# Performance work log

Measured on AMD Instinct MI355X. Metric: run time of the kernel, lower is better.

Reference implementation:

```python
import jax, jax.numpy as jnp
import numpy as np
from jax import lax

B, T, C_IN = 64, 1000, 12
D_MODEL, D_STATE, D_CONV, EXPAND = 128, 16, 4, 2
D_INNER = EXPAND * D_MODEL          # 256
DT_RANK = (D_MODEL + 15) // 16      # ceil(d_model/16) = 8
NUM_CLASSES = 5


def setup_inputs() -> dict:
    key = jax.random.key(0)
    ks = jax.random.split(key, 12)
    s = 0.05
    f = jnp.float32
    return {
        "x": jax.random.normal(ks[0], (B, T, C_IN), f),
        # input projection Linear(C_IN, D_MODEL) with bias
        "ip_w": jax.random.normal(ks[1], (D_MODEL, C_IN), f) * s,
        "ip_b": jnp.zeros((D_MODEL,), f),
        # Mamba block params (mamba_ssm layout)
        "in_proj_w": jax.random.normal(ks[2], (2 * D_INNER, D_MODEL), f) * s,
        "conv_w": jax.random.normal(ks[3], (D_INNER, D_CONV), f) * s,
        "conv_b": jnp.zeros((D_INNER,), f),
        "x_proj_w": jax.random.normal(ks[4], (DT_RANK + 2 * D_STATE, D_INNER), f) * s,
        "dt_proj_w": jax.random.normal(ks[5], (D_INNER, DT_RANK), f) * s,
        "dt_proj_b": jax.random.uniform(ks[6], (D_INNER,), f, -4.0, -2.0),  # softplus -> small positive dt
        "A_log": jnp.log(jnp.tile(jnp.arange(1, D_STATE + 1, dtype=f), (D_INNER, 1))),
        "D_skip": jnp.ones((D_INNER,), f),
        "out_proj_w": jax.random.normal(ks[7], (D_MODEL, D_INNER), f) * s,
        # classifier head: Linear(128,64) -> ReLU -> Linear(64,5)
        "fc1_w": jax.random.normal(ks[8], (64, D_MODEL), f) * s,
        "fc1_b": jnp.zeros((64,), f),
        "fc2_w": jax.random.normal(ks[9], (NUM_CLASSES, 64), f) * s,
        "fc2_b": jnp.zeros((NUM_CLASSES,), f),
    }


def _silu(x):
    return x * jax.nn.sigmoid(x)


def _mamba(h, in_proj_w, conv_w, conv_b, x_proj_w, dt_proj_w, dt_proj_b,
           A_log, D_skip, out_proj_w):
    # h: (B, T, D_MODEL)
    xz = h @ in_proj_w.T                              # (B, T, 2*Di)
    xm, z = jnp.split(xz, 2, axis=-1)
    # depthwise causal conv over time (pad left d_conv-1)
    xp = jnp.pad(xm, ((0, 0), (D_CONV - 1, 0), (0, 0)))
    rhs = conv_w.T[:, None, :]                        # (d_conv, 1, Di)
    xc = lax.conv_general_dilated(
        xp, rhs, (1,), 'VALID',
        dimension_numbers=('NHC', 'HIO', 'NHC'),
        feature_group_count=D_INNER) + conv_b
    u = _silu(xc)                                     # (B, T, Di)
    dbc = u @ x_proj_w.T                              # (B, T, dt_rank + 2N)
    dt = dbc[..., :DT_RANK]
    Bm = dbc[..., DT_RANK:DT_RANK + D_STATE]          # (B, T, N)
    Cm = dbc[..., DT_RANK + D_STATE:]                 # (B, T, N)
    delta = jax.nn.softplus(dt @ dt_proj_w.T + dt_proj_b)  # (B, T, Di)
    A = -jnp.exp(A_log)                               # (Di, N)

    def step(hst, inp):
        d_t, b_t, c_t, u_t = inp                      # (B,Di),(B,N),(B,N),(B,Di)
        dA = jnp.exp(d_t[..., None] * A)              # (B, Di, N)
        hst = dA * hst + (d_t * u_t)[..., None] * b_t[:, None, :]
        y_t = jnp.einsum('bdn,bn->bd', hst, c_t)
        return hst, y_t

    h0 = jnp.zeros((h.shape[0], D_INNER, D_STATE), h.dtype)
    _, ys = lax.scan(step, h0, (delta.transpose(1, 0, 2), Bm.transpose(1, 0, 2),
                                Cm.transpose(1, 0, 2), u.transpose(1, 0, 2)))
    y = ys.transpose(1, 0, 2) + u * D_skip            # (B, T, Di)
    y = y * _silu(z)
    return y @ out_proj_w.T                           # (B, T, D_MODEL)


def reference(x, ip_w, ip_b, in_proj_w, conv_w, conv_b, x_proj_w, dt_proj_w,
              dt_proj_b, A_log, D_skip, out_proj_w, fc1_w, fc1_b, fc2_w, fc2_b):
    h = x @ ip_w.T + ip_b                             # (B, T, D_MODEL)
    y = _mamba(h, in_proj_w, conv_w, conv_b, x_proj_w, dt_proj_w, dt_proj_b,
               A_log, D_skip, out_proj_w)
    last = y[:, -1, :]                                # (B, D_MODEL)
    hid = jax.nn.relu(last @ fc1_w.T + fc1_b)
    return hid @ fc2_w.T + fc2_b                      # (B, NUM_CLASSES)
```

## Files before the change

### kernel.cpp

```cpp
#include <hip/hip_runtime.h>
#include <cstddef>

#define T_LEN 1000
#define B_SZ 64
#define C_IN_ 12
#define D_MODEL_ 128
#define D_INNER_ 256
#define D_STATE_ 16
#define DT_RANK_ 8
#define N_CLS 5
#define NCH 5
#define CT4 50

typedef __attribute__((ext_vector_type(8))) short bf16x8;
typedef __attribute__((ext_vector_type(8))) unsigned short u16x8;
typedef __attribute__((ext_vector_type(4))) float f32x4;

__device__ __forceinline__ float fast_exp2(float x) {
#if __has_builtin(__builtin_amdgcn_exp2f)
  return __builtin_amdgcn_exp2f(x);
#else
  float r; asm volatile("v_exp_f32 %0, %1" : "=v"(r) : "v"(x)); return r;
#endif
}
__device__ __forceinline__ float fast_log2(float x) {
#if __has_builtin(__builtin_amdgcn_logf)
  return __builtin_amdgcn_logf(x);
#else
  float r; asm volatile("v_log_f32 %0, %1" : "=v"(r) : "v"(x)); return r;
#endif
}
__device__ __forceinline__ float fast_rcp(float x) {
#if __has_builtin(__builtin_amdgcn_rcpf)
  return __builtin_amdgcn_rcpf(x);
#else
  float r; asm volatile("v_rcp_f32 %0, %1" : "=v"(r) : "v"(x)); return r;
#endif
}
__device__ __forceinline__ float silu_f(float x) {
  float den = 1.f + fast_exp2(-x * 1.4426950408889634f);
  return x * fast_rcp(den);
}
__device__ __forceinline__ float softplus_f(float x) {
  const float L = 1.4426950408889634f, iL = 0.6931471805599453f;
  float e = fast_exp2(-fabsf(x) * L);
  float l = fast_log2(1.f + e) * iL;
  return fmaxf(x, 0.f) + l;
}
__device__ __forceinline__ unsigned short f2bf(float f) {
  unsigned u = __builtin_bit_cast(unsigned, f);
  u = u + 0x7FFFu + ((u >> 16) & 1u);
  return (unsigned short)(u >> 16);
}
__device__ __forceinline__ float bf2f(unsigned short h) {
  unsigned u = ((unsigned)h) << 16;
  return __builtin_bit_cast(float, u);
}

__global__ __launch_bounds__(256) void k0_prep(
    const float* __restrict__ x, const float* __restrict__ ip_w,
    const float* __restrict__ ip_b, const float* __restrict__ in_proj_w,
    char* __restrict__ h_pk, char* __restrict__ w_pk)
{
  __shared__ unsigned short pk_s[8192];
  __shared__ unsigned short pkw_s[32768];
  const int tid = threadIdx.x;

  if (blockIdx.x == 16) {
    if (blockIdx.y != 0) return;
    const int n = tid;
    for (int k = 0; k < D_MODEL_; ++k) {
      unsigned short v = f2bf(in_proj_w[(size_t)n * D_MODEL_ + k]);
      int off = ((n >> 4) * 4 + (k >> 5)) * 512 + ((k & 31) >> 3) * 128
              + (n & 15) * 8 + (k & 7);
      pkw_s[off] = v;
    }
    __syncthreads();
    const float4* s4 = (const float4*)pkw_s;
    float4* dst = (float4*)w_pk;
#pragma unroll
    for (int q = 0; q < 16; ++q) dst[tid * 16 + q] = s4[tid * 16 + q];
    return;
  }

  const int tile4 = blockIdx.x;
  const int b = blockIdx.y;
  const int rl = tid & 63;
  const int kc = (tid >> 6) * 32;
  const int t = tile4 * 64 + rl;

  float xr[C_IN_] = {0.f, 0.f, 0.f, 0.f, 0.f, 0.f, 0.f, 0.f, 0.f, 0.f, 0.f, 0.f};
  const bool valid = (t < T_LEN);
  if (valid) {
    const float4* xp = (const float4*)(x + ((size_t)b * T_LEN + t) * C_IN_);
    float4 v0 = xp[0], v1 = xp[1], v2 = xp[2];
    xr[0] = v0.x; xr[1] = v0.y; xr[2] = v0.z;  xr[3] = v0.w;
    xr[4] = v1.x; xr[5] = v1.y; xr[6] = v1.z;  xr[7] = v1.w;
    xr[8] = v2.x; xr[9] = v2.y; xr[10] = v2.z; xr[11] = v2.w;
  }
  for (int kk = 0; kk < 32; ++kk) {
    const int k = kc + kk;
    unsigned short v = 0;
    if (valid) {
      float acc = ip_b[k];
      const float* wr = ip_w + k * C_IN_;
#pragma unroll
      for (int c = 0; c < C_IN_; ++c) acc += xr[c] * wr[c];
      v = f2bf(acc);
    }
    int off = (rl >> 4) * 2048 + (k >> 5) * 512 + ((k & 31) >> 3) * 128
            + (rl & 15) * 8 + (k & 7);
    pk_s[off] = v;
  }
  __syncthreads();
  const float4* s4 = (const float4*)pk_s;
  float4* dst = (float4*)(h_pk + (size_t)(b * 64 + tile4 * 4) * 4096);
#pragma unroll
  for (int q = 0; q < 4; ++q) dst[tid * 4 + q] = s4[tid * 4 + q];
}

__global__ __launch_bounds__(256) void k1_u(
    const char* __restrict__ h_pk, const char* __restrict__ w_pk,
    const float* __restrict__ conv_w, const float* __restrict__ conv_b,
    float* __restrict__ u_out)
{
  __shared__ float xm[67][260];

  const int tile = blockIdx.x;
  const int b    = blockIdx.y;
  const int t0   = tile * 64;
  const int tid  = threadIdx.x;
  const int w    = tid >> 6;
  const int l    = tid & 63;

  {
    const char* achunk = h_pk + (size_t)(b * 64 + tile * 4 + w) * 4096;
    bf16x8 a0 = *(const bf16x8*)(achunk + 0 * 1024 + l * 16);
    bf16x8 a1 = *(const bf16x8*)(achunk + 1 * 1024 + l * 16);
    bf16x8 a2 = *(const bf16x8*)(achunk + 2 * 1024 + l * 16);
    bf16x8 a3 = *(const bf16x8*)(achunk + 3 * 1024 + l * 16);

    const int row_l = w * 16 + (l >> 4) * 4;
#pragma unroll
    for (int nt = 0; nt < 16; ++nt) {
      const char* wb = w_pk + (size_t)nt * 4096 + l * 16;
      bf16x8 b0 = *(const bf16x8*)(wb + 0 * 1024);
      bf16x8 b1 = *(const bf16x8*)(wb + 1 * 1024);
      bf16x8 b2 = *(const bf16x8*)(wb + 2 * 1024);
      bf16x8 b3 = *(const bf16x8*)(wb + 3 * 1024);
      f32x4 acc = {0.f, 0.f, 0.f, 0.f};
      acc = __builtin_amdgcn_mfma_f32_16x16x32_bf16(a0, b0, acc, 0, 0, 0);
      acc = __builtin_amdgcn_mfma_f32_16x16x32_bf16(a1, b1, acc, 0, 0, 0);
      acc = __builtin_amdgcn_mfma_f32_16x16x32_bf16(a2, b2, acc, 0, 0, 0);
      acc = __builtin_amdgcn_mfma_f32_16x16x32_bf16(a3, b3, acc, 0, 0, 0);
      const int col = nt * 16 + (l & 15);
#pragma unroll
      for (int r = 0; r < 4; ++r)
        xm[3 + row_l + r][col] = acc[r];
    }
  }

  {
    const int n = tid;
    float hac[3] = {0.f, 0.f, 0.f};
    if (tile > 0) {
      const char* wrow = w_pk + (size_t)(n >> 4) * 4096 + (n & 15) * 16;
#pragma unroll
      for (int kt = 0; kt < 4; ++kt)
#pragma unroll
        for (int lg = 0; lg < 4; ++lg) {
          u16x8 wv = *(const u16x8*)(wrow + kt * 1024 + lg * 256);
#pragma unroll
          for (int r = 0; r < 3; ++r) {
            const int t = t0 - 3 + r;
            const char* hc = h_pk + (size_t)(b * 64 + (t >> 4)) * 4096;
            u16x8 hv = *(const u16x8*)(hc + kt * 1024 + lg * 256 + (t & 15) * 16);
#pragma unroll
            for (int j = 0; j < 8; ++j) hac[r] += bf2f(hv[j]) * bf2f(wv[j]);
          }
        }
    }
#pragma unroll
    for (int r = 0; r < 3; ++r) xm[r][n] = hac[r];
  }
  __syncthreads();

  {
    const int n = tid;
    const float4 cw = *(const float4*)&conv_w[n * 4];
    const float  cb = conv_b[n];
    float x0 = xm[0][n], x1 = xm[1][n], x2 = xm[2][n];
    for (int i = 0; i < 64; ++i) {
      const int t = t0 + i;
      float x3 = xm[3 + i][n];
      if (t < T_LEN) {
        float s = cb + x0 * cw.x + x1 * cw.y + x2 * cw.z + x3 * cw.w;
        u_out[(((size_t)b * T_LEN + t) << 8) + n] = silu_f(s);
      }
      x0 = x1; x1 = x2; x2 = x3;
    }
  }
}

__global__ __launch_bounds__(256) void k3_delta(
    const float* __restrict__ u, const float* __restrict__ x_proj_w,
    const float* __restrict__ dt_proj_w, const float* __restrict__ dt_proj_b,
    float* __restrict__ pk_delta, float* __restrict__ pk_du,
    float* __restrict__ pk_bm, float* __restrict__ u_last)
{
  __shared__ float4 xp4[24][65];
  __shared__ float dt_s[64][9];
  __shared__ float bm_s[64][17];

  const int row0 = blockIdx.x * 64;
  const int tid = threadIdx.x;

  for (int f = tid; f < 24 * 64; f += 256) {
    int c = f >> 6, k4 = f & 63;
    xp4[c][k4] = *(const float4*)&x_proj_w[(size_t)c * 256 + k4 * 4];
  }
  const float4 w0 = *(const float4*)&dt_proj_w[(size_t)tid * 8];
  const float4 w1 = *(const float4*)&dt_proj_w[(size_t)tid * 8 + 4];
  const float bias = dt_proj_b[tid];
  __syncthreads();

  {
    const int r2 = tid >> 3, cg = tid & 7;
    const int ra = 2 * r2;
    const float4* ua4 = (const float4*)(u + (size_t)(row0 + ra) * 256);
    const float4* ub4 = (const float4*)(u + (size_t)(row0 + ra + 1) * 256);
    float a0 = 0.f, a1 = 0.f, a2 = 0.f, b0 = 0.f, b1 = 0.f, b2 = 0.f;
    for (int k4 = 0; k4 < 64; ++k4) {
      float4 a = ua4[k4], bb = ub4[k4];
      float4 q0 = xp4[cg * 3 + 0][k4];
      float4 q1 = xp4[cg * 3 + 1][k4];
      float4 q2 = xp4[cg * 3 + 2][k4];
      a0 += a.x * q0.x + a.y * q0.y + a.z * q0.z + a.w * q0.w;
      a1 += a.x * q1.x + a.y * q1.y + a.z * q1.z + a.w * q1.w;
      a2 += a.x * q2.x + a.y * q2.y + a.z * q2.z + a.w * q2.w;
      b0 += bb.x * q0.x + bb.y * q0.y + bb.z * q0.z + bb.w * q0.w;
      b1 += bb.x * q1.x + bb.y * q1.y + bb.z * q1.z + bb.w * q1.w;
      b2 += bb.x * q2.x + bb.y * q2.y + bb.z * q2.z + bb.w * q2.w;
    }
    float va[2][3] = {{a0, a1, a2}, {b0, b1, b2}};
#pragma unroll
    for (int rr = 0; rr < 2; ++rr)
#pragma unroll
      for (int c = 0; c < 3; ++c) {
        int col = cg * 3 + c;
        int row = ra + rr;
        if (col < 8) dt_s[row][col] = va[rr][c];
        else bm_s[row][col - 8] = va[rr][c];
      }
  }
  __syncthreads();

  for (int g = 0; g < 8; ++g) {
    float dd[8], uu[8];
#pragma unroll
    for (int j = 0; j < 8; ++j) {
      int r = g * 8 + j;
      float pre = bias
        + dt_s[r][0] * w0.x + dt_s[r][1] * w0.y + dt_s[r][2] * w0.z + dt_s[r][3] * w0.w
        + dt_s[r][4] * w1.x + dt_s[r][5] * w1.y + dt_s[r][6] * w1.z + dt_s[r][7] * w1.w;
      float dlt = softplus_f(pre);
      size_t o = (size_t)(row0 + r) * 256 + tid;
      float uv = u[o];
      dd[j] = dlt;
      uu[j] = dlt * uv;
      int rowg = row0 + r;
      if ((rowg - (rowg / 1000) * 1000) == 999)
        u_last[(rowg / 1000) * 256 + tid] = uv;
    }
    int row = row0 + g * 8;
    int bb_ = row / 1000;
    int t   = row - bb_ * 1000;
    size_t base = (((size_t)bb_ * 250 + (t >> 2)) * 256 + tid) * 4;
    *(float4*)&pk_delta[base]        = make_float4(dd[0], dd[1], dd[2], dd[3]);
    *(float4*)&pk_delta[base + 1024] = make_float4(dd[4], dd[5], dd[6], dd[7]);
    *(float4*)&pk_du[base]           = make_float4(uu[0], uu[1], uu[2], uu[3]);
    *(float4*)&pk_du[base + 1024]    = make_float4(uu[4], uu[5], uu[6], uu[7]);
  }
  if (tid < 16) {
    for (int g = 0; g < 8; ++g) {
      float pb[8];
#pragma unroll
      for (int j = 0; j < 8; ++j) pb[j] = bm_s[g * 8 + j][tid];
      int row = row0 + g * 8;
      int bb_ = row / 1000;
      int t   = row - bb_ * 1000;
      size_t base = (((size_t)bb_ * 250 + (t >> 2)) * 16 + tid) * 4;
      *(float4*)&pk_bm[base]      = make_float4(pb[0], pb[1], pb[2], pb[3]);
      *(float4*)&pk_bm[base + 64] = make_float4(pb[4], pb[5], pb[6], pb[7]);
    }
  }
}

__global__ __launch_bounds__(256) void k4_scan(
    const float* __restrict__ pk_delta, const float* __restrict__ pk_du,
    const float* __restrict__ pk_bm, const float* __restrict__ A_log,
    float* __restrict__ Qb, float* __restrict__ Pb)
{
  const int d0 = blockIdx.x * 16;
  const int b  = blockIdx.y;
  const int c  = blockIdx.z;
  const int tid = threadIdx.x;
  const int dl = tid >> 4;
  const int n  = tid & 15;
  const int d  = d0 + dl;

  const float A2 = -expf(A_log[(size_t)d * 16 + n]) * 1.4426950408889634f;
  float s = 0.f, sum = 0.f;

  const float* dp = pk_delta + ((size_t)b * 250 * 256 + d) * 4 + (size_t)c * CT4 * 1024;
  const float* xp = pk_du    + ((size_t)b * 250 * 256 + d) * 4 + (size_t)c * CT4 * 1024;
  const float* bp = pk_bm    + ((size_t)b * 250 * 16 + n) * 4 + (size_t)c * CT4 * 64;

  float4 dv = *(const float4*)dp;
  float4 xv = *(const float4*)xp;
  float4 bv = *(const float4*)bp;
  for (int i = 0; i < CT4 - 1; ++i) {
    float4 dvn = *(const float4*)(dp + (size_t)(i + 1) * 1024);
    float4 xvn = *(const float4*)(xp + (size_t)(i + 1) * 1024);
    float4 bvn = *(const float4*)(bp + (size_t)(i + 1) * 64);
    sum += (dv.x + dv.y) + (dv.z + dv.w);
    s = fast_exp2(dv.x * A2) * s + xv.x * bv.x;
    s = fast_exp2(dv.y * A2) * s + xv.y * bv.y;
    s = fast_exp2(dv.z * A2) * s + xv.z * bv.z;
    s = fast_exp2(dv.w * A2) * s + xv.w * bv.w;
    dv = dvn; xv = xvn; bv = bvn;
  }
  sum += (dv.x + dv.y) + (dv.z + dv.w);
  s = fast_exp2(dv.x * A2) * s + xv.x * bv.x;
  s = fast_exp2(dv.y * A2) * s + xv.y * bv.y;
  s = fast_exp2(dv.z * A2) * s + xv.z * bv.z;
  s = fast_exp2(dv.w * A2) * s + xv.w * bv.w;

  const size_t o = (size_t)c * 262144 + (size_t)b * 4096 + (size_t)d0 * 16 + tid;
  Qb[o] = s;
  Pb[o] = fast_exp2(A2 * sum);
}

__global__ __launch_bounds__(256) void k4b_combine(
    const float* __restrict__ Qb, const float* __restrict__ Pb,
    float* __restrict__ state_out)
{
  const size_t g = (size_t)blockIdx.x * 256 + threadIdx.x;
  float s = Qb[g];
#pragma unroll
  for (int c = 1; c < NCH; ++c)
    s = Qb[(size_t)c * 262144 + g] + Pb[(size_t)c * 262144 + g] * s;
  state_out[g] = s;
}

__global__ __launch_bounds__(256) void k5_head(
    const float* __restrict__ x, const float* __restrict__ ip_w,
    const float* __restrict__ ip_b, const float* __restrict__ in_proj_w,
    const float* __restrict__ x_proj_w, const float* __restrict__ u_last,
    const float* __restrict__ state, const float* __restrict__ D_skip,
    const float* __restrict__ out_proj_w, const float* __restrict__ fc1_w,
    const float* __restrict__ fc1_b, const float* __restrict__ fc2_w,
    const float* __restrict__ fc2_b, float* __restrict__ out)
{
  const int b = blockIdx.x, tid = threadIdx.x;
  __shared__ float hl[128], ul[256], zs[256], cm[16], yv[256], ov[128], hid[64];
  if (tid < 128) {
    float acc = ip_b[tid];
    const float* xr = x + ((size_t)b * T_LEN + (T_LEN - 1)) * C_IN_;
#pragma unroll
    for (int c = 0; c < C_IN_; ++c) acc += xr[c] * ip_w[tid * C_IN_ + c];
    hl[tid] = acc;
  }
  ul[tid] = u_last[b * 256 + tid];
  __syncthreads();
  {
    float acc = 0.f;
    const float4* wv = (const float4*)(in_proj_w + (size_t)(256 + tid) * 128);
    const float4* h4 = (const float4*)hl;
    for (int k = 0; k < 32; ++k) {
      float4 a = wv[k], c = h4[k];
      acc += c.x * a.x + c.y * a.y + c.z * a.z + c.w * a.w;
    }
    zs[tid] = silu_f(acc);
  }
  if (tid < 16) {
    float acc = 0.f;
    const float4* wv = (const float4*)(x_proj_w + (size_t)(24 + tid) * 256);
    const float4* u4 = (const float4*)ul;
    for (int k = 0; k < 64; ++k) {
      float4 a = wv[k], c = u4[k];
      acc += c.x * a.x + c.y * a.y + c.z * a.z + c.w * a.w;
    }
    cm[tid] = acc;
  }
  __syncthreads();
  {
    const float* st = state + ((size_t)b * 256 + tid) * 16;
    float acc = 0.f;
#pragma unroll
    for (int n = 0; n < 16; ++n) acc += st[n] * cm[n];
    yv[tid] = (acc + ul[tid] * D_skip[tid]) * zs[tid];
  }
  __syncthreads();
  if (tid < 128) {
    float acc = 0.f;
    const float4* wv = (const float4*)(out_proj_w + (size_t)tid * 256);
    const float4* y4 = (const float4*)yv;
    for (int k = 0; k < 64; ++k) {
      float4 a = wv[k], c = y4[k];
      acc += c.x * a.x + c.y * a.y + c.z * a.z + c.w * a.w;
    }
    ov[tid] = acc;
  }
  __syncthreads();
  if (tid < 64) {
    float acc = fc1_b[tid];
    const float4* wv = (const float4*)(fc1_w + (size_t)tid * 128);
    const float4* o4 = (const float4*)ov;
    for (int k = 0; k < 32; ++k) {
      float4 a = wv[k], c = o4[k];
      acc += c.x * a.x + c.y * a.y + c.z * a.z + c.w * a.w;
    }
    hid[tid] = fmaxf(acc, 0.f);
  }
  __syncthreads();
  if (tid < N_CLS) {
    float acc = fc2_b[tid];
    const float* wv = fc2_w + (size_t)tid * 64;
    for (int k = 0; k < 64; ++k) acc += hid[k] * wv[k];
    out[b * N_CLS + tid] = acc;
  }
}

extern "C" void kernel_launch(void* const* d_in, const int* in_sizes, int n_in,
                              void* d_out, int out_size, void* d_ws, size_t ws_size,
                              hipStream_t stream) {
  (void)in_sizes; (void)n_in; (void)out_size; (void)ws_size;
  const float* x         = (const float*)d_in[0];
  const float* ip_w      = (const float*)d_in[1];
  const float* ip_b      = (const float*)d_in[2];
  const float* in_proj_w = (const float*)d_in[3];
  const float* conv_w    = (const float*)d_in[4];
  const float* conv_b    = (const float*)d_in[5];
  const float* x_proj_w  = (const float*)d_in[6];
  const float* dt_proj_w = (const float*)d_in[7];
  const float* dt_proj_b = (const float*)d_in[8];
  const float* A_log     = (const float*)d_in[9];
  const float* D_skip    = (const float*)d_in[10];
  const float* out_proj_w= (const float*)d_in[11];
  const float* fc1_w     = (const float*)d_in[12];
  const float* fc1_b     = (const float*)d_in[13];
  const float* fc2_w     = (const float*)d_in[14];
  const float* fc2_b     = (const float*)d_in[15];
  float* out = (float*)d_out;

  float* u      = (float*)d_ws;
  float* delta  = u + (size_t)16384000;
  float* du     = delta + (size_t)16384000;
  float* bm     = du + (size_t)16384000;
  float* state  = bm + (size_t)1024000;
  float* u_last = state + (size_t)262144;
  char* h_pk = (char*)delta;
  char* w_pk = h_pk + (size_t)64 * 64 * 4096;
  float* Qb  = u;
  float* Pb  = u + (size_t)2000000;

  k0_prep<<<dim3(17, 64), 256, 0, stream>>>(x, ip_w, ip_b, in_proj_w, h_pk, w_pk);
  k1_u<<<dim3(16, 64), 256, 0, stream>>>(h_pk, w_pk, conv_w, conv_b, u);
  k3_delta<<<1000, 256, 0, stream>>>(u, x_proj_w, dt_proj_w, dt_proj_b,
                                     delta, du, bm, u_last);
  k4_scan<<<dim3(16, 64, NCH), 256, 0, stream>>>(delta, du, bm, A_log, Qb, Pb);
  k4b_combine<<<1024, 256, 0, stream>>>(Qb, Pb, state);
  k5_head<<<64, 256, 0, stream>>>(x, ip_w, ip_b, in_proj_w, x_proj_w, u_last, state,
                                  D_skip, out_proj_w, fc1_w, fc1_b, fc2_w, fc2_b, out);
}
```

Baseline: 219.7 us.

## Fuse conv/SiLU with x_proj and delta computation, deepen scan prefetch

Merges the u-producing kernel with the delta/B projection kernel so u stays in shared memory instead of round-tripping through a 64 MB global buffer. x_proj weights are now read directly from global memory rather than staged in LDS. The scan loop now prefetches two float4 groups per iteration instead of one, giving more loads in flight. The workspace layout is reorganised because u no longer exists.

Result: slower. 263.7 us (+20.0%).

```diff
diff --git a/kernel.cpp b/kernel.cpp
--- a/kernel.cpp
+++ b/kernel.cpp
@@ -10,7 +10,7 @@
 #define DT_RANK_ 8
 #define N_CLS 5
 #define NCH 5
-#define CT4 50
+#define CT8 25
 
 typedef __attribute__((ext_vector_type(8))) short bf16x8;
 typedef __attribute__((ext_vector_type(8))) unsigned short u16x8;
@@ -119,12 +119,17 @@
   for (int q = 0; q < 4; ++q) dst[tid * 4 + q] = s4[tid * 4 + q];
 }
 
-__global__ __launch_bounds__(256) void k1_u(
+__global__ __launch_bounds__(256) void k1_fused(
     const char* __restrict__ h_pk, const char* __restrict__ w_pk,
     const float* __restrict__ conv_w, const float* __restrict__ conv_b,
-    float* __restrict__ u_out)
+    const float* __restrict__ x_proj_w, const float* __restrict__ dt_proj_w,
+    const float* __restrict__ dt_proj_b,
+    float* __restrict__ pk_delta, float* __restrict__ pk_du,
+    float* __restrict__ pk_bm, float* __restrict__ u_last)
 {
   __shared__ float xm[67][260];
+  __shared__ float dt_s[64][9];
+  __shared__ float bm_s[64][17];
 
   const int tile = blockIdx.x;
   const int b    = blockIdx.y;
@@ -132,6 +137,10 @@
   const int tid  = threadIdx.x;
   const int w    = tid >> 6;
   const int l    = tid & 63;
+
+  const float4 w0 = *(const float4*)&dt_proj_w[(size_t)tid * 8];
+  const float4 w1 = *(const float4*)&dt_proj_w[(size_t)tid * 8 + 4];
+  const float bias = dt_proj_b[tid];
 
   {
     const char* achunk = h_pk + (size_t)(b * 64 + tile * 4 + w) * 4096;
@@ -191,50 +200,28 @@
     const float  cb = conv_b[n];
     float x0 = xm[0][n], x1 = xm[1][n], x2 = xm[2][n];
     for (int i = 0; i < 64; ++i) {
-      const int t = t0 + i;
       float x3 = xm[3 + i][n];
-      if (t < T_LEN) {
-        float s = cb + x0 * cw.x + x1 * cw.y + x2 * cw.z + x3 * cw.w;
-        u_out[(((size_t)b * T_LEN + t) << 8) + n] = silu_f(s);
-      }
+      float s = cb + x0 * cw.x + x1 * cw.y + x2 * cw.z + x3 * cw.w;
+      float uv = silu_f(s);
+      xm[i][n] = uv;
+      if (t0 + i == T_LEN - 1) u_last[b * 256 + n] = uv;
       x0 = x1; x1 = x2; x2 = x3;
     }
   }
-}
-
-__global__ __launch_bounds__(256) void k3_delta(
-    const float* __restrict__ u, const float* __restrict__ x_proj_w,
-    const float* __restrict__ dt_proj_w, const float* __restrict__ dt_proj_b,
-    float* __restrict__ pk_delta, float* __restrict__ pk_du,
-    float* __restrict__ pk_bm, float* __restrict__ u_last)
-{
-  __shared__ float4 xp4[24][65];
-  __shared__ float dt_s[64][9];
-  __shared__ float bm_s[64][17];
-
-  const int row0 = blockIdx.x * 64;
-  const int tid = threadIdx.x;
-
-  for (int f = tid; f < 24 * 64; f += 256) {
-    int c = f >> 6, k4 = f & 63;
-    xp4[c][k4] = *(const float4*)&x_proj_w[(size_t)c * 256 + k4 * 4];
-  }
-  const float4 w0 = *(const float4*)&dt_proj_w[(size_t)tid * 8];
-  const float4 w1 = *(const float4*)&dt_proj_w[(size_t)tid * 8 + 4];
-  const float bias = dt_proj_b[tid];
   __syncthreads();
 
   {
     const int r2 = tid >> 3, cg = tid & 7;
     const int ra = 2 * r2;
-    const float4* ua4 = (const float4*)(u + (size_t)(row0 + ra) * 256);
-    const float4* ub4 = (const float4*)(u + (size_t)(row0 + ra + 1) * 256);
+    const float4* ua4 = (const float4*)&xm[ra][0];
+    const float4* ub4 = (const float4*)&xm[ra + 1][0];
     float a0 = 0.f, a1 = 0.f, a2 = 0.f, b0 = 0.f, b1 = 0.f, b2 = 0.f;
+    const float4* q0p = (const float4*)&x_proj_w[(size_t)(cg * 3 + 0) * 256];
+    const float4* q1p = (const float4*)&x_proj_w[(size_t)(cg * 3 + 1) * 256];
+    const float4* q2p = (const float4*)&x_proj_w[(size_t)(cg * 3 + 2) * 256];
     for (int k4 = 0; k4 < 64; ++k4) {
       float4 a = ua4[k4], bb = ub4[k4];
-      float4 q0 = xp4[cg * 3 + 0][k4];
-      float4 q1 = xp4[cg * 3 + 1][k4];
-      float4 q2 = xp4[cg * 3 + 2][k4];
+      float4 q0 = q0p[k4], q1 = q1p[k4], q2 = q2p[k4];
       a0 += a.x * q0.x + a.y * q0.y + a.z * q0.z + a.w * q0.w;
       a1 += a.x * q1.x + a.y * q1.y + a.z * q1.z + a.w * q1.w;
       a2 += a.x * q2.x + a.y * q2.y + a.z * q2.z + a.w * q2.w;
@@ -256,6 +243,7 @@
   __syncthreads();
 
   for (int g = 0; g < 8; ++g) {
+    if (t0 + g * 8 >= T_LEN) break;
     float dd[8], uu[8];
 #pragma unroll
     for (int j = 0; j < 8; ++j) {
@@ -264,18 +252,11 @@
         + dt_s[r][0] * w0.x + dt_s[r][1] * w0.y + dt_s[r][2] * w0.z + dt_s[r][3] * w0.w
         + dt_s[r][4] * w1.x + dt_s[r][5] * w1.y + dt_s[r][6] * w1.z + dt_s[r][7] * w1.w;
       float dlt = softplus_f(pre);
-      size_t o = (size_t)(row0 + r) * 256 + tid;
-      float uv = u[o];
       dd[j] = dlt;
-      uu[j] = dlt * uv;
-      int rowg = row0 + r;
-      if ((rowg - (rowg / 1000) * 1000) == 999)
-        u_last[(rowg / 1000) * 256 + tid] = uv;
-    }
-    int row = row0 + g * 8;
-    int bb_ = row / 1000;
-    int t   = row - bb_ * 1000;
-    size_t base = (((size_t)bb_ * 250 + (t >> 2)) * 256 + tid) * 4;
+      uu[j] = dlt * xm[r][tid];
+    }
+    int t = t0 + g * 8;
+    size_t base = (((size_t)b * 250 + (t >> 2)) * 256 + tid) * 4;
     *(float4*)&pk_delta[base]        = make_float4(dd[0], dd[1], dd[2], dd[3]);
     *(float4*)&pk_delta[base + 1024] = make_float4(dd[4], dd[5], dd[6], dd[7]);
     *(float4*)&pk_du[base]           = make_float4(uu[0], uu[1], uu[2], uu[3]);
@@ -283,13 +264,12 @@
   }
   if (tid < 16) {
     for (int g = 0; g < 8; ++g) {
+      if (t0 + g * 8 >= T_LEN) break;
       float pb[8];
 #pragma unroll
       for (int j = 0; j < 8; ++j) pb[j] = bm_s[g * 8 + j][tid];
-      int row = row0 + g * 8;
-      int bb_ = row / 1000;
-      int t   = row - bb_ * 1000;
-      size_t base = (((size_t)bb_ * 250 + (t >> 2)) * 16 + tid) * 4;
+      int t = t0 + g * 8;
+      size_t base = (((size_t)b * 250 + (t >> 2)) * 16 + tid) * 4;
       *(float4*)&pk_bm[base]      = make_float4(pb[0], pb[1], pb[2], pb[3]);
       *(float4*)&pk_bm[base + 64] = make_float4(pb[4], pb[5], pb[6], pb[7]);
     }
@@ -312,29 +292,42 @@
   const float A2 = -expf(A_log[(size_t)d * 16 + n]) * 1.4426950408889634f;
   float s = 0.f, sum = 0.f;
 
-  const float* dp = pk_delta + ((size_t)b * 250 * 256 + d) * 4 + (size_t)c * CT4 * 1024;
-  const float* xp = pk_du    + ((size_t)b * 250 * 256 + d) * 4 + (size_t)c * CT4 * 1024;
-  const float* bp = pk_bm    + ((size_t)b * 250 * 16 + n) * 4 + (size_t)c * CT4 * 64;
-
-  float4 dv = *(const float4*)dp;
-  float4 xv = *(const float4*)xp;
-  float4 bv = *(const float4*)bp;
-  for (int i = 0; i < CT4 - 1; ++i) {
-    float4 dvn = *(const float4*)(dp + (size_t)(i + 1) * 1024);
-    float4 xvn = *(const float4*)(xp + (size_t)(i + 1) * 1024);
-    float4 bvn = *(const float4*)(bp + (size_t)(i + 1) * 64);
-    sum += (dv.x + dv.y) + (dv.z + dv.w);
-    s = fast_exp2(dv.x * A2) * s + xv.x * bv.x;
-    s = fast_exp2(dv.y * A2) * s + xv.y * bv.y;
-    s = fast_exp2(dv.z * A2) * s + xv.z * bv.z;
-    s = fast_exp2(dv.w * A2) * s + xv.w * bv.w;
-    dv = dvn; xv = xvn; bv = bvn;
-  }
-  sum += (dv.x + dv.y) + (dv.z + dv.w);
-  s = fast_exp2(dv.x * A2) * s + xv.x * bv.x;
-  s = fast_exp2(dv.y * A2) * s + xv.y * bv.y;
-  s = fast_exp2(dv.z * A2) * s + xv.z * bv.z;
-  s = fast_exp2(dv.w * A2) * s + xv.w * bv.w;
+  const float* dp = pk_delta + ((size_t)b * 250 * 256 + d) * 4 + (size_t)c * 50 * 1024;
+  const float* xp = pk_du    + ((size_t)b * 250 * 256 + d) * 4 + (size_t)c * 50 * 1024;
+  const float* bp = pk_bm    + ((size_t)b * 250 * 16 + n) * 4 + (size_t)c * 50 * 64;
+
+  float4 dA = *(const float4*)dp;
+  float4 dB = *(const float4*)(dp + 1024);
+  float4 xA = *(const float4*)xp;
+  float4 xB = *(const float4*)(xp + 1024);
+  float4 bA = *(const float4*)bp;
+  float4 bB = *(const float4*)(bp + 64);
+
+  for (int it = 0; it < CT8; ++it) {
+    const int nx = (it < CT8 - 1) ? (2 * it + 2) : (2 * it);
+    const float* dpn = dp + (size_t)nx * 1024;
+    const float* xpn = xp + (size_t)nx * 1024;
+    const float* bpn = bp + (size_t)nx * 64;
+    float4 dN0 = *(const float4*)dpn;
+    float4 dN1 = *(const float4*)(dpn + 1024);
+    float4 xN0 = *(const float4*)xpn;
+    float4 xN1 = *(const float4*)(xpn + 1024);
+    float4 bN0 = *(const float4*)bpn;
+    float4 bN1 = *(const float4*)(bpn + 64);
+
+    sum += (dA.x + dA.y) + (dA.z + dA.w);
+    s = fast_exp2(dA.x * A2) * s + xA.x * bA.x;
+    s = fast_exp2(dA.y * A2) * s + xA.y * bA.y;
+    s = fast_exp2(dA.z * A2) * s + xA.z * bA.z;
+    s = fast_exp2(dA.w * A2) * s + xA.w * bA.w;
+    sum += (dB.x + dB.y) + (dB.z + dB.w);
+    s = fast_exp2(dB.x * A2) * s + xB.x * bB.x;
+    s = fast_exp2(dB.y * A2) * s + xB.y * bB.y;
+    s = fast_exp2(dB.z * A2) * s + xB.z * bB.z;
+    s = fast_exp2(dB.w * A2) * s + xB.w * bB.w;
+
+    dA = dN0; dB = dN1; xA = xN0; xB = xN1; bA = bN0; bB = bN1;
+  }
 
   const size_t o = (size_t)c * 262144 + (size_t)b * 4096 + (size_t)d0 * 16 + tid;
   Qb[o] = s;
@@ -454,22 +447,21 @@
   const float* fc2_b     = (const float*)d_in[15];
   float* out = (float*)d_out;
 
-  float* u      = (float*)d_ws;
-  float* delta  = u + (size_t)16384000;
-  float* du     = delta + (size_t)16384000;
-  float* bm     = du + (size_t)16384000;
-  float* state  = bm + (size_t)1024000;
-  float* u_last = state + (size_t)262144;
-  char* h_pk = (char*)delta;
-  char* w_pk = h_pk + (size_t)64 * 64 * 4096;
-  float* Qb  = u;
-  float* Pb  = u + (size_t)2000000;
+  float* pk_delta = (float*)d_ws;
+  float* pk_du    = pk_delta + (size_t)16384000;
+  float* pk_bm    = pk_du + (size_t)16384000;
+  float* state    = pk_bm + (size_t)1024000;
+  float* u_last   = state + (size_t)262144;
+  float* Qb       = u_last + (size_t)16384;
+  float* Pb       = Qb + (size_t)1310720;
+  char*  h_pk     = (char*)(Pb + (size_t)1310720);
+  char*  w_pk     = h_pk + (size_t)64 * 64 * 4096;
 
   k0_prep<<<dim3(17, 64), 256, 0, stream>>>(x, ip_w, ip_b, in_proj_w, h_pk, w_pk);
-  k1_u<<<dim3(16, 64), 256, 0, stream>>>(h_pk, w_pk, conv_w, conv_b, u);
-  k3_delta<<<1000, 256, 0, stream>>>(u, x_proj_w, dt_proj_w, dt_proj_b,
-                                     delta, du, bm, u_last);
-  k4_scan<<<dim3(16, 64, NCH), 256, 0, stream>>>(delta, du, bm, A_log, Qb, Pb);
+  k1_fused<<<dim3(16, 64), 256, 0, stream>>>(h_pk, w_pk, conv_w, conv_b,
+                                             x_proj_w, dt_proj_w, dt_proj_b,
+                                             pk_delta, pk_du, pk_bm, u_last);
+  k4_scan<<<dim3(16, 64, NCH), 256, 0, stream>>>(pk_delta, pk_du, pk_bm, A_log, Qb, Pb);
   k4b_combine<<<1024, 256, 0, stream>>>(Qb, Pb, state);
   k5_head<<<64, 256, 0, stream>>>(x, ip_w, ip_b, in_proj_w, x_proj_w, u_last, state,
                                   D_skip, out_proj_w, fc1_w, fc1_b, fc2_w, fc2_b, out);
```

## Store delta and du time-contiguous per channel and stage B in LDS for scan

Applied to the files above, without the earlier changes.

The delta and du buffers are now written time-major per (batch, channel) row instead of in 4-step packed blocks interleaved across channels. The scan kernel reads each channel's contiguous time run and keeps the B-matrix chunk in shared memory, and its 50-step loop is fully unrolled. The intent is to let the compiler issue many independent loads ahead, hiding memory latency in the serial recurrence. In exchange, loads within a wavefront are strided across lanes (16 lanes share a channel, and channels sit 4000 bytes apart), which may reduce coalescing in both the writer and the scan.

Measured after the change: 218.2 us. About the same (-0.7%).

```diff
diff --git a/kernel.cpp b/kernel.cpp
--- a/kernel.cpp
+++ b/kernel.cpp
@@ -10,7 +10,6 @@
 #define DT_RANK_ 8
 #define N_CLS 5
 #define NCH 5
-#define CT4 50
 
 typedef __attribute__((ext_vector_type(8))) short bf16x8;
 typedef __attribute__((ext_vector_type(8))) unsigned short u16x8;
@@ -205,7 +204,7 @@
 __global__ __launch_bounds__(256) void k3_delta(
     const float* __restrict__ u, const float* __restrict__ x_proj_w,
     const float* __restrict__ dt_proj_w, const float* __restrict__ dt_proj_b,
-    float* __restrict__ pk_delta, float* __restrict__ pk_du,
+    float* __restrict__ delta_T, float* __restrict__ du_T,
     float* __restrict__ pk_bm, float* __restrict__ u_last)
 {
   __shared__ float4 xp4[24][65];
@@ -275,11 +274,11 @@
     int row = row0 + g * 8;
     int bb_ = row / 1000;
     int t   = row - bb_ * 1000;
-    size_t base = (((size_t)bb_ * 250 + (t >> 2)) * 256 + tid) * 4;
-    *(float4*)&pk_delta[base]        = make_float4(dd[0], dd[1], dd[2], dd[3]);
-    *(float4*)&pk_delta[base + 1024] = make_float4(dd[4], dd[5], dd[6], dd[7]);
-    *(float4*)&pk_du[base]           = make_float4(uu[0], uu[1], uu[2], uu[3]);
-    *(float4*)&pk_du[base + 1024]    = make_float4(uu[4], uu[5], uu[6], uu[7]);
+    size_t rb = ((size_t)(bb_ * 256 + tid)) * 1000 + t;
+    *(float4*)&delta_T[rb]     = make_float4(dd[0], dd[1], dd[2], dd[3]);
+    *(float4*)&delta_T[rb + 4] = make_float4(dd[4], dd[5], dd[6], dd[7]);
+    *(float4*)&du_T[rb]        = make_float4(uu[0], uu[1], uu[2], uu[3]);
+    *(float4*)&du_T[rb + 4]    = make_float4(uu[4], uu[5], uu[6], uu[7]);
   }
   if (tid < 16) {
     for (int g = 0; g < 8; ++g) {
@@ -297,10 +296,12 @@
 }
 
 __global__ __launch_bounds__(256) void k4_scan(
-    const float* __restrict__ pk_delta, const float* __restrict__ pk_du,
+    const float* __restrict__ delta_T, const float* __restrict__ du_T,
     const float* __restrict__ pk_bm, const float* __restrict__ A_log,
     float* __restrict__ Qb, float* __restrict__ Pb)
 {
+  __shared__ float bs[50][16][4];
+
   const int d0 = blockIdx.x * 16;
   const int b  = blockIdx.y;
   const int c  = blockIdx.z;
@@ -309,32 +310,28 @@
   const int n  = tid & 15;
   const int d  = d0 + dl;
 
+  {
+    const float4* src = (const float4*)(pk_bm + ((size_t)b * 250 + (size_t)c * 50) * 64);
+    float4* dst = (float4*)bs;
+    for (int f = tid; f < 800; f += 256) dst[f] = src[f];
+  }
   const float A2 = -expf(A_log[(size_t)d * 16 + n]) * 1.4426950408889634f;
+  const float* dp = delta_T + ((size_t)(b * 256 + d)) * 1000 + c * 200;
+  const float* xp = du_T    + ((size_t)(b * 256 + d)) * 1000 + c * 200;
+  __syncthreads();
+
   float s = 0.f, sum = 0.f;
-
-  const float* dp = pk_delta + ((size_t)b * 250 * 256 + d) * 4 + (size_t)c * CT4 * 1024;
-  const float* xp = pk_du    + ((size_t)b * 250 * 256 + d) * 4 + (size_t)c * CT4 * 1024;
-  const float* bp = pk_bm    + ((size_t)b * 250 * 16 + n) * 4 + (size_t)c * CT4 * 64;
-
-  float4 dv = *(const float4*)dp;
-  float4 xv = *(const float4*)xp;
-  float4 bv = *(const float4*)bp;
-  for (int i = 0; i < CT4 - 1; ++i) {
-    float4 dvn = *(const float4*)(dp + (size_t)(i + 1) * 1024);
-    float4 xvn = *(const float4*)(xp + (size_t)(i + 1) * 1024);
-    float4 bvn = *(const float4*)(bp + (size_t)(i + 1) * 64);
+#pragma unroll
+  for (int i = 0; i < 50; ++i) {
+    float4 dv = *(const float4*)(dp + 4 * i);
+    float4 xv = *(const float4*)(xp + 4 * i);
+    float4 bv = *(const float4*)&bs[i][n][0];
     sum += (dv.x + dv.y) + (dv.z + dv.w);
     s = fast_exp2(dv.x * A2) * s + xv.x * bv.x;
     s = fast_exp2(dv.y * A2) * s + xv.y * bv.y;
     s = fast_exp2(dv.z * A2) * s + xv.z * bv.z;
     s = fast_exp2(dv.w * A2) * s + xv.w * bv.w;
-    dv = dvn; xv = xvn; bv = bvn;
-  }
-  sum += (dv.x + dv.y) + (dv.z + dv.w);
-  s = fast_exp2(dv.x * A2) * s + xv.x * bv.x;
-  s = fast_exp2(dv.y * A2) * s + xv.y * bv.y;
-  s = fast_exp2(dv.z * A2) * s + xv.z * bv.z;
-  s = fast_exp2(dv.w * A2) * s + xv.w * bv.w;
+  }
 
   const size_t o = (size_t)c * 262144 + (size_t)b * 4096 + (size_t)d0 * 16 + tid;
   Qb[o] = s;
@@ -454,13 +451,13 @@
   const float* fc2_b     = (const float*)d_in[15];
   float* out = (float*)d_out;
 
-  float* u      = (float*)d_ws;
-  float* delta  = u + (size_t)16384000;
-  float* du     = delta + (size_t)16384000;
-  float* bm     = du + (size_t)16384000;
-  float* state  = bm + (size_t)1024000;
-  float* u_last = state + (size_t)262144;
-  char* h_pk = (char*)delta;
+  float* u       = (float*)d_ws;
+  float* delta_T = u + (size_t)16384000;
+  float* du_T    = delta_T + (size_t)16384000;
+  float* pk_bm   = du_T + (size_t)16384000;
+  float* state   = pk_bm + (size_t)1024000;
+  float* u_last  = state + (size_t)262144;
+  char* h_pk = (char*)delta_T;
   char* w_pk = h_pk + (size_t)64 * 64 * 4096;
   float* Qb  = u;
   float* Pb  = u + (size_t)2000000;
@@ -468,8 +465,8 @@
   k0_prep<<<dim3(17, 64), 256, 0, stream>>>(x, ip_w, ip_b, in_proj_w, h_pk, w_pk);
   k1_u<<<dim3(16, 64), 256, 0, stream>>>(h_pk, w_pk, conv_w, conv_b, u);
   k3_delta<<<1000, 256, 0, stream>>>(u, x_proj_w, dt_proj_w, dt_proj_b,
-                                     delta, du, bm, u_last);
-  k4_scan<<<dim3(16, 64, NCH), 256, 0, stream>>>(delta, du, bm, A_log, Qb, Pb);
+                                     delta_T, du_T, pk_bm, u_last);
+  k4_scan<<<dim3(16, 64, NCH), 256, 0, stream>>>(delta_T, du_T, pk_bm, A_log, Qb, Pb);
   k4b_combine<<<1024, 256, 0, stream>>>(Qb, Pb, state);
   k5_head<<<64, 256, 0, stream>>>(x, ip_w, ip_b, in_proj_w, x_proj_w, u_last, state,
                                   D_skip, out_proj_w, fc1_w, fc1_b, fc2_w, fc2_b, out);
```
